# Performance work log

Hardware: AMD Instinct MI355X
Metric: run time of the kernel (lower is better)

## Reference

```python
import jax, jax.numpy as jnp
import numpy as np

N_NODES = 20000
N_EDGES = 320000
IN_FEATS = 128
HID = 32
HEADS1 = 8
OUT_FEATS = 64


def _segment_softmax(logits, seg, num_segments):
    # logits: [E, H] grouped by destination node `seg`
    m = jax.ops.segment_max(logits, seg, num_segments=num_segments)  # [N, H]
    e = jnp.exp(logits - m[seg])
    s = jax.ops.segment_sum(e, seg, num_segments=num_segments)  # [N, H]
    return e / (s[seg] + 1e-16)


def _gat_conv(x, edge_index, W, a_src, a_dst, b, heads, ch, concat, neg_slope):
    # x: [N, F_in]; W: [F_in, heads*ch]; a_src/a_dst: [heads, ch]; b: [heads*ch] or [ch]
    N = x.shape[0]
    # add self-loops (PyG GATConv default add_self_loops=True)
    loop = jnp.arange(N, dtype=edge_index.dtype)
    src = jnp.concatenate([edge_index[0], loop])
    dst = jnp.concatenate([edge_index[1], loop])

    h = (x @ W).reshape(N, heads, ch)                      # [N, H, C]
    alpha_src = jnp.einsum('nhc,hc->nh', h, a_src)          # [N, H]
    alpha_dst = jnp.einsum('nhc,hc->nh', h, a_dst)          # [N, H]

    alpha = jax.nn.leaky_relu(alpha_src[src] + alpha_dst[dst], neg_slope)  # [E', H]
    alpha = _segment_softmax(alpha, dst, N)                 # [E', H]

    msg = h[src] * alpha[:, :, None]                        # [E', H, C]
    out = jax.ops.segment_sum(msg, dst, num_segments=N)     # [N, H, C]

    if concat:
        out = out.reshape(N, heads * ch)
    else:
        out = out.mean(axis=1)
    return out + b


def setup_inputs() -> dict:
    key = jax.random.key(0)
    ks = jax.random.split(key, 10)
    x = jax.random.normal(ks[0], (N_NODES, IN_FEATS), dtype=jnp.float32)
    edge_index = jax.random.randint(ks[1], (2, N_EDGES), 0, N_NODES, dtype=jnp.int32)

    def glorot(k, shape):
        fan = sum(shape[-2:]) if len(shape) > 1 else shape[-1]
        return jax.random.normal(k, shape, dtype=jnp.float32) * jnp.sqrt(2.0 / fan)

    W1 = glorot(ks[2], (IN_FEATS, HEADS1 * HID))
    a_src1 = glorot(ks[3], (HEADS1, HID))
    a_dst1 = glorot(ks[4], (HEADS1, HID))
    b1 = jnp.zeros((HEADS1 * HID,), dtype=jnp.float32)
    W2 = glorot(ks[5], (HEADS1 * HID, OUT_FEATS))
    a_src2 = glorot(ks[6], (1, OUT_FEATS))
    a_dst2 = glorot(ks[7], (1, OUT_FEATS))
    b2 = jnp.zeros((OUT_FEATS,), dtype=jnp.float32)
    return {"x": x, "W1": W1, "a_src1": a_src1, "a_dst1": a_dst1, "b1": b1,
            "W2": W2, "a_src2": a_src2, "a_dst2": a_dst2, "b2": b2,
            "edge_index": edge_index}


def reference(x, W1, a_src1, a_dst1, b1, W2, a_src2, a_dst2, b2, edge_index):
    h = _gat_conv(x, edge_index, W1, a_src1, a_dst1, b1,
                  heads=HEADS1, ch=HID, concat=True, neg_slope=0.2)
    h = jax.nn.leaky_relu(h, 0.01)  # F.leaky_relu default slope
    out = _gat_conv(h, edge_index, W2, a_src2, a_dst2, b2,
                    heads=1, ch=OUT_FEATS, concat=False, neg_slope=0.2)
    return out
```

## Files before the change

### kernel.cpp

```cpp
#include <hip/hip_runtime.h>
#include <hip/hip_fp16.h>

#define NN 20000
#define NE 320000
#define EP (NE + NN)
#define FIN 128
#define HEADS 8
#define HID 32
#define C1 256
#define C2 64
#define CAP 64

typedef _Float16 f16;
typedef __attribute__((ext_vector_type(8))) _Float16 f16x8;
typedef __attribute__((ext_vector_type(4))) _Float16 f16x4;
typedef __attribute__((ext_vector_type(4))) float f32x4;

#define PREP_T (FIN * C1 + C1 * C2)
#define PREP_BLKS ((PREP_T + 255) / 256)
#define EB ((EP + 255) / 256)

__global__ void k_zero(int* __restrict__ p, int n) {
    int i = blockIdx.x * 256 + threadIdx.x;
    if (i < n) p[i] = 0;
}

__global__ void k_prepbucket(const float* __restrict__ W1, const float* __restrict__ W2,
                             f16* __restrict__ W1T, f16* __restrict__ W2T,
                             const int* __restrict__ ei, int* __restrict__ cnt,
                             int* __restrict__ bucket) {
    const int b = blockIdx.x;
    if (b < PREP_BLKS) {
        int j = b * 256 + threadIdx.x;
        if (j < FIN * C1) {
            int k = j >> 8, n = j & 255;
            W1T[n * FIN + k] = (f16)W1[j];
            return;
        }
        j -= FIN * C1;
        if (j < C1 * C2) {
            int k = j >> 6, n = j & 63;
            W2T[n * C1 + k] = (f16)W2[j];
        }
        return;
    }
    int e = (b - PREP_BLKS) * 256 + threadIdx.x;
    if (e >= EP) return;
    int src, dst;
    if (e < NE) { src = ei[e]; dst = ei[NE + e]; }
    else { src = dst = e - NE; }
    int pos = atomicAdd(&cnt[dst], 1);
    if (pos < CAP) bucket[(size_t)dst * CAP + pos] = src;
}

__device__ __forceinline__ int swz(int row, int kb) {
    return (row * 64 + kb) ^ ((row & 7) << 4);
}

template <typename AT, typename OT, int MODE>
__global__ __launch_bounds__(256) void k_mgemm(const AT* __restrict__ A,
                                               const f16* __restrict__ BT,
                                               OT* __restrict__ C, int M, int N, int K,
                                               const float* __restrict__ a_src,
                                               const float* __restrict__ a_dst,
                                               float* __restrict__ as_o,
                                               float* __restrict__ ad_o) {
    __shared__ char lds[8192];
    __shared__ float sred[64][2];
    char* as = lds;
    char* bs = lds + 4096;
    const int t = threadIdx.x;
    const int bm = blockIdx.y * 64;
    const int bn = blockIdx.x * 64;
    const int srow = t >> 2;
    const int skb = (t & 3) * 16;
    const int sk8 = (t & 3) * 8;
    const int l = t & 63;
    const int w = t >> 6;
    const int wr = (w >> 1) * 32, wc = (w & 1) * 32;
    const int lr = l & 15, lg = l >> 4;
    f32x4 acc00 = {}, acc01 = {}, acc10 = {}, acc11 = {};
    const bool arow_ok = (bm + srow) < M;
    const AT* gA = A + (size_t)(bm + srow) * K + sk8;
    const f16* gB = BT + (size_t)(bn + srow) * K + sk8;
    for (int k0 = 0; k0 < K; k0 += 32) {
        f16x8 av = {};
        if (arow_ok) {
            if constexpr (sizeof(AT) == 2) {
                av = *(const f16x8*)(gA + k0);
            } else {
                float4 f0 = *(const float4*)(gA + k0);
                float4 f1 = *(const float4*)(gA + k0 + 4);
                av = {(_Float16)f0.x, (_Float16)f0.y, (_Float16)f0.z, (_Float16)f0.w,
                      (_Float16)f1.x, (_Float16)f1.y, (_Float16)f1.z, (_Float16)f1.w};
            }
        }
        f16x8 bv = *(const f16x8*)(gB + k0);
        __syncthreads();
        *(f16x8*)(as + swz(srow, skb)) = av;
        *(f16x8*)(bs + swz(srow, skb)) = bv;
        __syncthreads();
        f16x8 a0 = *(f16x8*)(as + swz(wr + lr, lg * 16));
        f16x8 a1 = *(f16x8*)(as + swz(wr + 16 + lr, lg * 16));
        f16x8 b0 = *(f16x8*)(bs + swz(wc + lr, lg * 16));
        f16x8 b1 = *(f16x8*)(bs + swz(wc + 16 + lr, lg * 16));
        acc00 = __builtin_amdgcn_mfma_f32_16x16x32_f16(a0, b0, acc00, 0, 0, 0);
        acc01 = __builtin_amdgcn_mfma_f32_16x16x32_f16(a0, b1, acc01, 0, 0, 0);
        acc10 = __builtin_amdgcn_mfma_f32_16x16x32_f16(a1, b0, acc10, 0, 0, 0);
        acc11 = __builtin_amdgcn_mfma_f32_16x16x32_f16(a1, b1, acc11, 0, 0, 0);
    }
    const int crow0 = bm + wr + lg * 4;
    const int ccol0 = bn + wc + lr;
#pragma unroll
    for (int r = 0; r < 4; ++r) {
        int r0 = crow0 + r;
        if (r0 < M) {
            C[(size_t)r0 * N + ccol0] = (OT)acc00[r];
            C[(size_t)r0 * N + ccol0 + 16] = (OT)acc01[r];
        }
        int r1 = r0 + 16;
        if (r1 < M) {
            C[(size_t)r1 * N + ccol0] = (OT)acc10[r];
            C[(size_t)r1 * N + ccol0 + 16] = (OT)acc11[r];
        }
    }
    if constexpr (MODE == 1) {
        const float av0 = a_src[ccol0], av1 = a_src[ccol0 + 16];
        const float dv0 = a_dst[ccol0], dv1 = a_dst[ccol0 + 16];
        const int head = (bn + wc) >> 5;
#pragma unroll
        for (int r = 0; r < 4; ++r) {
            float ps0 = acc00[r] * av0 + acc01[r] * av1;
            float pd0 = acc00[r] * dv0 + acc01[r] * dv1;
            float ps1 = acc10[r] * av0 + acc11[r] * av1;
            float pd1 = acc10[r] * dv0 + acc11[r] * dv1;
#pragma unroll
            for (int off = 1; off < 16; off <<= 1) {
                ps0 += __shfl_xor(ps0, off, 16);
                pd0 += __shfl_xor(pd0, off, 16);
                ps1 += __shfl_xor(ps1, off, 16);
                pd1 += __shfl_xor(pd1, off, 16);
            }
            if (lr == 0) {
                int row0 = crow0 + r, row1 = row0 + 16;
                if (row0 < M) { as_o[row0 * HEADS + head] = ps0; ad_o[row0 * HEADS + head] = pd0; }
                if (row1 < M) { as_o[row1 * HEADS + head] = ps1; ad_o[row1 * HEADS + head] = pd1; }
            }
        }
    }
    if constexpr (MODE == 2) {
        const float av0 = a_src[ccol0], av1 = a_src[ccol0 + 16];
        const float dv0 = a_dst[ccol0], dv1 = a_dst[ccol0 + 16];
        float psl[8], pdl[8];
#pragma unroll
        for (int r = 0; r < 4; ++r) {
            psl[r]     = acc00[r] * av0 + acc01[r] * av1;
            pdl[r]     = acc00[r] * dv0 + acc01[r] * dv1;
            psl[r + 4] = acc10[r] * av0 + acc11[r] * av1;
            pdl[r + 4] = acc10[r] * dv0 + acc11[r] * dv1;
        }
#pragma unroll
        for (int i = 0; i < 8; ++i) {
#pragma unroll
            for (int off = 1; off < 16; off <<= 1) {
                psl[i] += __shfl_xor(psl[i], off, 16);
                pdl[i] += __shfl_xor(pdl[i], off, 16);
            }
        }
        if (((w & 1) == 0) && lr == 0) {
#pragma unroll
            for (int r = 0; r < 4; ++r) {
                int row0 = wr + lg * 4 + r, row1 = row0 + 16;
                sred[row0][0] = psl[r];     sred[row0][1] = pdl[r];
                sred[row1][0] = psl[r + 4]; sred[row1][1] = pdl[r + 4];
            }
        }
        __syncthreads();
        if (((w & 1) == 1) && lr == 0) {
#pragma unroll
            for (int r = 0; r < 4; ++r) {
                int row0 = wr + lg * 4 + r, row1 = row0 + 16;
                int g0 = bm + row0, g1 = bm + row1;
                if (g0 < M) { as_o[g0] = sred[row0][0] + psl[r];     ad_o[g0] = sred[row0][1] + pdl[r]; }
                if (g1 < M) { as_o[g1] = sred[row1][0] + psl[r + 4]; ad_o[g1] = sred[row1][1] + pdl[r + 4]; }
            }
        }
    }
}

__global__ void k_agg1(const f16* __restrict__ h1h, const float* __restrict__ as1,
                       const float* __restrict__ ad1, const int* __restrict__ cnt,
                       const int* __restrict__ bucket, const float* __restrict__ b1,
                       f16* __restrict__ out) {
    const int l = threadIdx.x & 31;
    const int n = (blockIdx.x << 3) + (threadIdx.x >> 5);
    const int h = l >> 2;
    int deg = cnt[n];
    deg = (deg < CAP) ? deg : CAP;
    const int* __restrict__ row = bucket + (size_t)n * CAP;
    const float adn = ad1[n * HEADS + h];
    float s = 0.f;
    float a[8] = {};
    for (int j = 0; j < deg; j += 8) {
        const int jd = deg - j;
        const int4 ia = *(const int4*)(row + j);
        const int4 ib = *(const int4*)(row + j + 4);
        int idx[8] = {ia.x, ia.y, ia.z, ia.w, ib.x, ib.y, ib.z, ib.w};
#pragma unroll
        for (int k = 1; k < 8; ++k) idx[k] = (k < jd) ? idx[k] : idx[0];
        f16x8 q[8];
        float wv[8];
#pragma unroll
        for (int k = 0; k < 8; ++k) q[k] = ((const f16x8*)(h1h + (size_t)idx[k] * C1))[l];
#pragma unroll
        for (int k = 0; k < 8; ++k) {
            float xk = as1[idx[k] * HEADS + h] + adn;
            xk = (xk > 0.f) ? xk : 0.2f * xk;
            float e = expf(xk);
            wv[k] = (k < jd) ? e : 0.f;
        }
#pragma unroll
        for (int k = 0; k < 8; ++k) {
            s += wv[k];
#pragma unroll
            for (int c = 0; c < 8; ++c) a[c] += (float)q[k][c] * wv[k];
        }
    }
    const float inv = 1.f / (s + 1e-16f);
    const float4 bv0 = ((const float4*)b1)[2 * l];
    const float4 bv1 = ((const float4*)b1)[2 * l + 1];
    float o[8];
    o[0] = a[0] * inv + bv0.x; o[1] = a[1] * inv + bv0.y;
    o[2] = a[2] * inv + bv0.z; o[3] = a[3] * inv + bv0.w;
    o[4] = a[4] * inv + bv1.x; o[5] = a[5] * inv + bv1.y;
    o[6] = a[6] * inv + bv1.z; o[7] = a[7] * inv + bv1.w;
    f16x8 o16;
#pragma unroll
    for (int c = 0; c < 8; ++c) {
        float v = (o[c] > 0.f) ? o[c] : 0.01f * o[c];
        o16[c] = (_Float16)v;
    }
    ((f16x8*)(out + (size_t)n * C1))[l] = o16;
}

__global__ void k_agg2(const f16* __restrict__ h2h, const float* __restrict__ as2,
                       const float* __restrict__ ad2, const int* __restrict__ cnt,
                       const int* __restrict__ bucket, const float* __restrict__ b2,
                       float* __restrict__ out) {
    const int g = threadIdx.x & 15;
    const int n = (blockIdx.x << 4) + (threadIdx.x >> 4);
    int deg = cnt[n];
    deg = (deg < CAP) ? deg : CAP;
    const int* __restrict__ row = bucket + (size_t)n * CAP;
    const float adn = ad2[n];
    float s = 0.f;
    float a0 = 0.f, a1 = 0.f, a2 = 0.f, a3 = 0.f;
    for (int j = 0; j < deg; j += 8) {
        const int jd = deg - j;
        const int4 ia = *(const int4*)(row + j);
        const int4 ib = *(const int4*)(row + j + 4);
        int idx[8] = {ia.x, ia.y, ia.z, ia.w, ib.x, ib.y, ib.z, ib.w};
#pragma unroll
        for (int k = 1; k < 8; ++k) idx[k] = (k < jd) ? idx[k] : idx[0];
        f16x4 q[8];
        float wv[8];
#pragma unroll
        for (int k = 0; k < 8; ++k) q[k] = ((const f16x4*)(h2h + (size_t)idx[k] * C2))[g];
#pragma unroll
        for (int k = 0; k < 8; ++k) {
            float xk = as2[idx[k]] + adn;
            xk = (xk > 0.f) ? xk : 0.2f * xk;
            float e = expf(xk);
            wv[k] = (k < jd) ? e : 0.f;
        }
#pragma unroll
        for (int k = 0; k < 8; ++k) {
            s += wv[k];
            a0 += (float)q[k][0] * wv[k];
            a1 += (float)q[k][1] * wv[k];
            a2 += (float)q[k][2] * wv[k];
            a3 += (float)q[k][3] * wv[k];
        }
    }
    const float inv = 1.f / (s + 1e-16f);
    const float4 bv = ((const float4*)b2)[g];
    float4 o;
    o.x = a0 * inv + bv.x;
    o.y = a1 * inv + bv.y;
    o.z = a2 * inv + bv.z;
    o.w = a3 * inv + bv.w;
    ((float4*)(out + (size_t)n * C2))[g] = o;
}

extern "C" void kernel_launch(void* const* d_in, const int* in_sizes, int n_in,
                              void* d_out, int out_size, void* d_ws, size_t ws_size,
                              hipStream_t stream) {
    const float* x      = (const float*)d_in[0];
    const float* W1     = (const float*)d_in[1];
    const float* a_src1 = (const float*)d_in[2];
    const float* a_dst1 = (const float*)d_in[3];
    const float* b1     = (const float*)d_in[4];
    const float* W2     = (const float*)d_in[5];
    const float* a_src2 = (const float*)d_in[6];
    const float* a_dst2 = (const float*)d_in[7];
    const float* b2     = (const float*)d_in[8];
    const int*   ei     = (const int*)d_in[9];
    float* out = (float*)d_out;

    char* ws = (char*)d_ws;
    size_t off = 0;
    auto alloc = [&](size_t bytes) {
        void* p = ws + off;
        off += (bytes + 255) & ~(size_t)255;
        return p;
    };
    f16*  W1T    = (f16*)alloc((size_t)C1 * FIN * 2);
    f16*  W2T    = (f16*)alloc((size_t)C2 * C1 * 2);
    f16*  h1h    = (f16*)alloc((size_t)NN * C1 * 2);
    f16*  hl2h   = (f16*)alloc((size_t)NN * C1 * 2);
    f16*  h2h    = (f16*)alloc((size_t)NN * C2 * 2);
    float* as1   = (float*)alloc((size_t)NN * HEADS * 4);
    float* ad1   = (float*)alloc((size_t)NN * HEADS * 4);
    float* as2   = (float*)alloc((size_t)NN * 4);
    float* ad2   = (float*)alloc((size_t)NN * 4);
    int*   cnt   = (int*)alloc((size_t)NN * 4);
    int*   bucket= (int*)alloc((size_t)NN * CAP * 4);

    k_zero<<<(NN + 255) / 256, 256, 0, stream>>>(cnt, NN);

    k_prepbucket<<<PREP_BLKS + EB, 256, 0, stream>>>(W1, W2, W1T, W2T, ei, cnt, bucket);

    k_mgemm<float, f16, 1><<<dim3(C1 / 64, (NN + 63) / 64), 256, 0, stream>>>(
        x, W1T, h1h, NN, C1, FIN, a_src1, a_dst1, as1, ad1);
    k_agg1<<<NN / 8, 256, 0, stream>>>(h1h, as1, ad1, cnt, bucket, b1, hl2h);

    k_mgemm<f16, f16, 2><<<dim3(C2 / 64, (NN + 63) / 64), 256, 0, stream>>>(
        hl2h, W2T, h2h, NN, C2, C1, a_src2, a_dst2, as2, ad2);
    k_agg2<<<NN / 16, 256, 0, stream>>>(h2h, as2, ad2, cnt, bucket, b2, out);
}
```

Before: 89.84 us.

## Fuse first GEMM with bucketing kernel and split edge loops across lanes in aggregation

Merges the layer-1 GEMM, W2 transpose and edge bucketing into one launch, removing a kernel and the W1 transpose by reading W1 as fp32 directly with strided loads. The GEMM and the bucketing blocks now run concurrently in one grid. Both aggregation kernels assign two lane groups per node, each processing alternate chunks of 8 neighbours, then combine partial sums with cross-lane shuffles, which doubles memory-level parallelism per node. The strided uncoalesced W1 reads in the GEMM inner loop and the idle upper half during the epilogue are the costs.

```diff
diff --git a/kernel.cpp b/kernel.cpp
--- a/kernel.cpp
+++ b/kernel.cpp
@@ -16,8 +16,8 @@
 typedef __attribute__((ext_vector_type(4))) _Float16 f16x4;
 typedef __attribute__((ext_vector_type(4))) float f32x4;
 
-#define PREP_T (FIN * C1 + C1 * C2)
-#define PREP_BLKS ((PREP_T + 255) / 256)
+#define GB1 (4 * ((NN + 63) / 64))
+#define PREP2_BLKS ((C1 * C2 + 255) / 256)
 #define EB ((EP + 255) / 256)
 
 __global__ void k_zero(int* __restrict__ p, int n) {
@@ -25,53 +25,25 @@
     if (i < n) p[i] = 0;
 }
 
-__global__ void k_prepbucket(const float* __restrict__ W1, const float* __restrict__ W2,
-                             f16* __restrict__ W1T, f16* __restrict__ W2T,
-                             const int* __restrict__ ei, int* __restrict__ cnt,
-                             int* __restrict__ bucket) {
-    const int b = blockIdx.x;
-    if (b < PREP_BLKS) {
-        int j = b * 256 + threadIdx.x;
-        if (j < FIN * C1) {
-            int k = j >> 8, n = j & 255;
-            W1T[n * FIN + k] = (f16)W1[j];
-            return;
-        }
-        j -= FIN * C1;
-        if (j < C1 * C2) {
-            int k = j >> 6, n = j & 63;
-            W2T[n * C1 + k] = (f16)W2[j];
-        }
-        return;
-    }
-    int e = (b - PREP_BLKS) * 256 + threadIdx.x;
-    if (e >= EP) return;
-    int src, dst;
-    if (e < NE) { src = ei[e]; dst = ei[NE + e]; }
-    else { src = dst = e - NE; }
-    int pos = atomicAdd(&cnt[dst], 1);
-    if (pos < CAP) bucket[(size_t)dst * CAP + pos] = src;
-}
-
 __device__ __forceinline__ int swz(int row, int kb) {
     return (row * 64 + kb) ^ ((row & 7) << 4);
 }
 
-template <typename AT, typename OT, int MODE>
-__global__ __launch_bounds__(256) void k_mgemm(const AT* __restrict__ A,
-                                               const f16* __restrict__ BT,
-                                               OT* __restrict__ C, int M, int N, int K,
-                                               const float* __restrict__ a_src,
-                                               const float* __restrict__ a_dst,
-                                               float* __restrict__ as_o,
-                                               float* __restrict__ ad_o) {
+template <typename AT, bool BF32, typename OT, int MODE>
+__device__ __forceinline__ void mgemm_body(int bx, int by, const AT* __restrict__ A,
+                                           const void* __restrict__ Bp,
+                                           OT* __restrict__ C, int M, int N, int K,
+                                           const float* __restrict__ a_src,
+                                           const float* __restrict__ a_dst,
+                                           float* __restrict__ as_o,
+                                           float* __restrict__ ad_o) {
     __shared__ char lds[8192];
     __shared__ float sred[64][2];
     char* as = lds;
     char* bs = lds + 4096;
     const int t = threadIdx.x;
-    const int bm = blockIdx.y * 64;
-    const int bn = blockIdx.x * 64;
+    const int bm = by * 64;
+    const int bn = bx * 64;
     const int srow = t >> 2;
     const int skb = (t & 3) * 16;
     const int sk8 = (t & 3) * 8;
@@ -82,7 +54,6 @@
     f32x4 acc00 = {}, acc01 = {}, acc10 = {}, acc11 = {};
     const bool arow_ok = (bm + srow) < M;
     const AT* gA = A + (size_t)(bm + srow) * K + sk8;
-    const f16* gB = BT + (size_t)(bn + srow) * K + sk8;
     for (int k0 = 0; k0 < K; k0 += 32) {
         f16x8 av = {};
         if (arow_ok) {
@@ -95,7 +66,16 @@
                       (_Float16)f1.x, (_Float16)f1.y, (_Float16)f1.z, (_Float16)f1.w};
             }
         }
-        f16x8 bv = *(const f16x8*)(gB + k0);
+        f16x8 bv;
+        if constexpr (BF32) {
+            const float* B = (const float*)Bp;
+#pragma unroll
+            for (int i = 0; i < 8; ++i)
+                bv[i] = (_Float16)B[(size_t)(k0 + sk8 + i) * N + bn + srow];
+        } else {
+            const f16* BT = (const f16*)Bp;
+            bv = *(const f16x8*)(BT + (size_t)(bn + srow) * K + sk8 + k0);
+        }
         __syncthreads();
         *(f16x8*)(as + swz(srow, skb)) = av;
         *(f16x8*)(bs + swz(srow, skb)) = bv;
@@ -188,30 +168,82 @@
     }
 }
 
+__global__ __launch_bounds__(256) void k_fused1(const float* __restrict__ x,
+                                                const float* __restrict__ W1,
+                                                const float* __restrict__ W2,
+                                                f16* __restrict__ W2T,
+                                                const int* __restrict__ ei,
+                                                int* __restrict__ cnt,
+                                                int* __restrict__ bucket,
+                                                f16* __restrict__ h1h,
+                                                const float* __restrict__ a_src1,
+                                                const float* __restrict__ a_dst1,
+                                                float* __restrict__ as1,
+                                                float* __restrict__ ad1) {
+    int b = blockIdx.x;
+    if (b < GB1) {
+        mgemm_body<float, true, f16, 1>(b & 3, b >> 2, x, W1, h1h, NN, C1, FIN,
+                                        a_src1, a_dst1, as1, ad1);
+        return;
+    }
+    b -= GB1;
+    if (b < PREP2_BLKS) {
+        int j = b * 256 + threadIdx.x;
+        if (j < C1 * C2) {
+            int k = j >> 6, n = j & 63;
+            W2T[n * C1 + k] = (f16)W2[j];
+        }
+        return;
+    }
+    b -= PREP2_BLKS;
+    int e = b * 256 + threadIdx.x;
+    if (e >= EP) return;
+    int src, dst;
+    if (e < NE) { src = ei[e]; dst = ei[NE + e]; }
+    else { src = dst = e - NE; }
+    int pos = atomicAdd(&cnt[dst], 1);
+    if (pos < CAP) bucket[(size_t)dst * CAP + pos] = src;
+}
+
+__global__ __launch_bounds__(256) void k_mgemm2(const f16* __restrict__ A,
+                                                const f16* __restrict__ BT,
+                                                f16* __restrict__ C,
+                                                const float* __restrict__ a_src,
+                                                const float* __restrict__ a_dst,
+                                                float* __restrict__ as_o,
+                                                float* __restrict__ ad_o) {
+    mgemm_body<f16, false, f16, 2>(blockIdx.x, blockIdx.y, A, BT, C, NN, C2, C1,
+                                   a_src, a_dst, as_o, ad_o);
+}
+
 __global__ void k_agg1(const f16* __restrict__ h1h, const float* __restrict__ as1,
                        const float* __restrict__ ad1, const int* __restrict__ cnt,
                        const int* __restrict__ bucket, const float* __restrict__ b1,
                        f16* __restrict__ out) {
-    const int l = threadIdx.x & 31;
-    const int n = (blockIdx.x << 3) + (threadIdx.x >> 5);
-    const int h = l >> 2;
+    const int l = threadIdx.x & 63;
+    const int n = (blockIdx.x << 2) + (threadIdx.x >> 6);
+    const int c = l & 31;
+    const int half = l >> 5;
+    const int h = c >> 2;
     int deg = cnt[n];
     deg = (deg < CAP) ? deg : CAP;
     const int* __restrict__ row = bucket + (size_t)n * CAP;
     const float adn = ad1[n * HEADS + h];
     float s = 0.f;
     float a[8] = {};
-    for (int j = 0; j < deg; j += 8) {
-        const int jd = deg - j;
-        const int4 ia = *(const int4*)(row + j);
-        const int4 ib = *(const int4*)(row + j + 4);
+    for (int b = 0;; ++b) {
+        const int j0 = 16 * b + 8 * half;
+        if (j0 >= deg) break;
+        const int jd = deg - j0;
+        const int4 ia = *(const int4*)(row + j0);
+        const int4 ib = *(const int4*)(row + j0 + 4);
         int idx[8] = {ia.x, ia.y, ia.z, ia.w, ib.x, ib.y, ib.z, ib.w};
 #pragma unroll
         for (int k = 1; k < 8; ++k) idx[k] = (k < jd) ? idx[k] : idx[0];
         f16x8 q[8];
         float wv[8];
 #pragma unroll
-        for (int k = 0; k < 8; ++k) q[k] = ((const f16x8*)(h1h + (size_t)idx[k] * C1))[l];
+        for (int k = 0; k < 8; ++k) q[k] = ((const f16x8*)(h1h + (size_t)idx[k] * C1))[c];
 #pragma unroll
         for (int k = 0; k < 8; ++k) {
             float xk = as1[idx[k] * HEADS + h] + adn;
@@ -223,49 +255,58 @@
         for (int k = 0; k < 8; ++k) {
             s += wv[k];
 #pragma unroll
-            for (int c = 0; c < 8; ++c) a[c] += (float)q[k][c] * wv[k];
-        }
-    }
-    const float inv = 1.f / (s + 1e-16f);
-    const float4 bv0 = ((const float4*)b1)[2 * l];
-    const float4 bv1 = ((const float4*)b1)[2 * l + 1];
-    float o[8];
-    o[0] = a[0] * inv + bv0.x; o[1] = a[1] * inv + bv0.y;
-    o[2] = a[2] * inv + bv0.z; o[3] = a[3] * inv + bv0.w;
-    o[4] = a[4] * inv + bv1.x; o[5] = a[5] * inv + bv1.y;
-    o[6] = a[6] * inv + bv1.z; o[7] = a[7] * inv + bv1.w;
-    f16x8 o16;
-#pragma unroll
-    for (int c = 0; c < 8; ++c) {
-        float v = (o[c] > 0.f) ? o[c] : 0.01f * o[c];
-        o16[c] = (_Float16)v;
-    }
-    ((f16x8*)(out + (size_t)n * C1))[l] = o16;
+            for (int cc = 0; cc < 8; ++cc) a[cc] += (float)q[k][cc] * wv[k];
+        }
+    }
+    s += __shfl_xor(s, 32, 64);
+#pragma unroll
+    for (int cc = 0; cc < 8; ++cc) a[cc] += __shfl_xor(a[cc], 32, 64);
+    if (half == 0) {
+        const float inv = 1.f / (s + 1e-16f);
+        const float4 bv0 = ((const float4*)b1)[2 * c];
+        const float4 bv1 = ((const float4*)b1)[2 * c + 1];
+        float o[8];
+        o[0] = a[0] * inv + bv0.x; o[1] = a[1] * inv + bv0.y;
+        o[2] = a[2] * inv + bv0.z; o[3] = a[3] * inv + bv0.w;
+        o[4] = a[4] * inv + bv1.x; o[5] = a[5] * inv + bv1.y;
+        o[6] = a[6] * inv + bv1.z; o[7] = a[7] * inv + bv1.w;
+        f16x8 o16;
+#pragma unroll
+        for (int cc = 0; cc < 8; ++cc) {
+            float v = (o[cc] > 0.f) ? o[cc] : 0.01f * o[cc];
+            o16[cc] = (_Float16)v;
+        }
+        ((f16x8*)(out + (size_t)n * C1))[c] = o16;
+    }
 }
 
 __global__ void k_agg2(const f16* __restrict__ h2h, const float* __restrict__ as2,
                        const float* __restrict__ ad2, const int* __restrict__ cnt,
                        const int* __restrict__ bucket, const float* __restrict__ b2,
                        float* __restrict__ out) {
-    const int g = threadIdx.x & 15;
-    const int n = (blockIdx.x << 4) + (threadIdx.x >> 4);
+    const int lw = threadIdx.x & 31;
+    const int n = (blockIdx.x << 3) + (threadIdx.x >> 5);
+    const int c = lw & 15;
+    const int half = lw >> 4;
     int deg = cnt[n];
     deg = (deg < CAP) ? deg : CAP;
     const int* __restrict__ row = bucket + (size_t)n * CAP;
     const float adn = ad2[n];
     float s = 0.f;
     float a0 = 0.f, a1 = 0.f, a2 = 0.f, a3 = 0.f;
-    for (int j = 0; j < deg; j += 8) {
-        const int jd = deg - j;
-        const int4 ia = *(const int4*)(row + j);
-        const int4 ib = *(const int4*)(row + j + 4);
+    for (int b = 0;; ++b) {
+        const int j0 = 16 * b + 8 * half;
+        if (j0 >= deg) break;
+        const int jd = deg - j0;
+        const int4 ia = *(const int4*)(row + j0);
+        const int4 ib = *(const int4*)(row + j0 + 4);
         int idx[8] = {ia.x, ia.y, ia.z, ia.w, ib.x, ib.y, ib.z, ib.w};
 #pragma unroll
         for (int k = 1; k < 8; ++k) idx[k] = (k < jd) ? idx[k] : idx[0];
         f16x4 q[8];
         float wv[8];
 #pragma unroll
-        for (int k = 0; k < 8; ++k) q[k] = ((const f16x4*)(h2h + (size_t)idx[k] * C2))[g];
+        for (int k = 0; k < 8; ++k) q[k] = ((const f16x4*)(h2h + (size_t)idx[k] * C2))[c];
 #pragma unroll
         for (int k = 0; k < 8; ++k) {
             float xk = as2[idx[k]] + adn;
@@ -282,14 +323,21 @@
             a3 += (float)q[k][3] * wv[k];
         }
     }
-    const float inv = 1.f / (s + 1e-16f);
-    const float4 bv = ((const float4*)b2)[g];
-    float4 o;
-    o.x = a0 * inv + bv.x;
-    o.y = a1 * inv + bv.y;
-    o.z = a2 * inv + bv.z;
-    o.w = a3 * inv + bv.w;
-    ((float4*)(out + (size_t)n * C2))[g] = o;
+    s  += __shfl_xor(s, 16, 32);
+    a0 += __shfl_xor(a0, 16, 32);
+    a1 += __shfl_xor(a1, 16, 32);
+    a2 += __shfl_xor(a2, 16, 32);
+    a3 += __shfl_xor(a3, 16, 32);
+    if (half == 0) {
+        const float inv = 1.f / (s + 1e-16f);
+        const float4 bv = ((const float4*)b2)[c];
+        float4 o;
+        o.x = a0 * inv + bv.x;
+        o.y = a1 * inv + bv.y;
+        o.z = a2 * inv + bv.z;
+        o.w = a3 * inv + bv.w;
+        ((float4*)(out + (size_t)n * C2))[c] = o;
+    }
 }
 
 extern "C" void kernel_launch(void* const* d_in, const int* in_sizes, int n_in,
@@ -314,7 +362,6 @@
         off += (bytes + 255) & ~(size_t)255;
         return p;
     };
-    f16*  W1T    = (f16*)alloc((size_t)C1 * FIN * 2);
     f16*  W2T    = (f16*)alloc((size_t)C2 * C1 * 2);
     f16*  h1h    = (f16*)alloc((size_t)NN * C1 * 2);
     f16*  hl2h   = (f16*)alloc((size_t)NN * C1 * 2);
@@ -328,13 +375,13 @@
 
     k_zero<<<(NN + 255) / 256, 256, 0, stream>>>(cnt, NN);
 
-    k_prepbucket<<<PREP_BLKS + EB, 256, 0, stream>>>(W1, W2, W1T, W2T, ei, cnt, bucket);
-
-    k_mgemm<float, f16, 1><<<dim3(C1 / 64, (NN + 63) / 64), 256, 0, stream>>>(
-        x, W1T, h1h, NN, C1, FIN, a_src1, a_dst1, as1, ad1);
-    k_agg1<<<NN / 8, 256, 0, stream>>>(h1h, as1, ad1, cnt, bucket, b1, hl2h);
-
-    k_mgemm<f16, f16, 2><<<dim3(C2 / 64, (NN + 63) / 64), 256, 0, stream>>>(
-        hl2h, W2T, h2h, NN, C2, C1, a_src2, a_dst2, as2, ad2);
-    k_agg2<<<NN / 16, 256, 0, stream>>>(h2h, as2, ad2, cnt, bucket, b2, out);
-}
+    k_fused1<<<GB1 + PREP2_BLKS + EB, 256, 0, stream>>>(
+        x, W1, W2, W2T, ei, cnt, bucket, h1h, a_src1, a_dst1, as1, ad1);
+
+    k_agg1<<<NN / 4, 256, 0, stream>>>(h1h, as1, ad1, cnt, bucket, b1, hl2h);
+
+    k_mgemm2<<<dim3(C2 / 64, (NN + 63) / 64), 256, 0, stream>>>(
+        hl2h, W2T, h2h, a_src2, a_dst2, as2, ad2);
+
+    k_agg2<<<NN / 8, 256, 0, stream>>>(h2h, as2, ad2, cnt, bucket, b2, out);
+}
```

Measured after the change: 80.18 us. 10.8% less time.
